# Optimization experiments

Measured on AMD Instinct MI355X. Metric: run time of the kernel, lower is better.

Reference implementation:

```python
import jax, jax.numpy as jnp
import numpy as np

N, E, H, ED = 20000, 320000, 256, 64  # nodes, edges, hidden_dim, edge_feature_dim


def setup_inputs() -> dict:
    key = jax.random.key(0)
    ks = jax.random.split(key, 12)

    def init_w(k, shape, fan_in):
        return (jax.random.normal(k, shape, jnp.float32) / np.sqrt(fan_in)).astype(jnp.float32)

    h = jax.random.normal(ks[0], (N, H), jnp.float32)
    edge_indices = jax.random.randint(ks[1], (2, E), 0, N, jnp.int32)
    edge_attr = jax.random.normal(ks[2], (E, ED), jnp.float32)

    din = 2 * H + ED  # edge_network input: [h[row], h[col], edge_attr]
    W1 = init_w(ks[3], (H, din), din)
    b1 = jnp.zeros((H,), jnp.float32)
    W2 = init_w(ks[4], (H, H), H)
    b2 = jnp.zeros((H,), jnp.float32)
    # GRUCell params, gate order (r, z, n) as in torch
    W_ih = init_w(ks[5], (3 * H, H), H)
    b_ih = jnp.zeros((3 * H,), jnp.float32)
    W_hh = init_w(ks[6], (3 * H, H), H)
    b_hh = jnp.zeros((3 * H,), jnp.float32)

    return {"h": h, "edge_indices": edge_indices, "edge_attr": edge_attr,
            "W1": W1, "b1": b1, "W2": W2, "b2": b2,
            "W_ih": W_ih, "b_ih": b_ih, "W_hh": W_hh, "b_hh": b_hh}


def reference(h, edge_indices, edge_attr, W1, b1, W2, b2, W_ih, b_ih, W_hh, b_hh):
    row, col = edge_indices[0], edge_indices[1]
    # message: edge_network MLP on [h[row], h[col], edge_attr]
    edge_in = jnp.concatenate([h[row], h[col], edge_attr], axis=-1)  # [E, 2H+ED]
    msg = jax.nn.relu(edge_in @ W1.T + b1) @ W2.T + b2               # [E, H]
    # scatter_add aggregation by destination node (row)
    agg = jax.ops.segment_sum(msg, row, num_segments=h.shape[0])     # [N, H]
    # GRUCell update: input=agg, hidden=h
    gx = agg @ W_ih.T + b_ih
    gh = h @ W_hh.T + b_hh
    xr, xz, xn = jnp.split(gx, 3, axis=-1)
    hr, hz, hn = jnp.split(gh, 3, axis=-1)
    r = jax.nn.sigmoid(xr + hr)
    z = jax.nn.sigmoid(xz + hz)
    n = jnp.tanh(xn + r * hn)
    h_new = (1.0 - z) * n + z * h
    return h_new  # dropout p=0.0 -> identity
```

## Files before the change

kernel.cpp:

```cpp
#include <hip/hip_runtime.h>
#include <math.h>

#define NN 20000
#define NE 320000
#define HD 256
#define EDIM 64
#define DIN 576
#define ASTRIDE 264

typedef __attribute__((ext_vector_type(4))) _Float16 h4;
typedef __attribute__((ext_vector_type(8))) _Float16 h8;
typedef __attribute__((ext_vector_type(4))) float f32x4;

__device__ _Float16 g_W1cf[16 * 2 * 64 * 8];
__device__ _Float16 g_W12f[32 * 8 * 64 * 8];
__device__ _Float16 g_Wrzf[32 * 16 * 64 * 8];
__device__ _Float16 g_Wnxf[16 * 8 * 64 * 8];
__device__ _Float16 g_Wnhf[16 * 8 * 64 * 8];
__device__ float    g_Wib2[768];
__device__ _Float16 g_pre[(size_t)NN * 512];
__device__ _Float16 g_hf[(size_t)NN * 256];
__device__ int      g_rowptr[NN + 1];
__device__ int      g_cursor[NN];
__device__ int      g_perm[NE];
__device__ int      g_prow[NE];
__device__ int      g_pcol[NE];

__device__ __forceinline__ h4 f2h4(float4 v) {
  return (h4){(_Float16)v.x, (_Float16)v.y, (_Float16)v.z, (_Float16)v.w};
}
__device__ __forceinline__ h8 f2h8(float4 a, float4 b) {
  return (h8){(_Float16)a.x, (_Float16)a.y, (_Float16)a.z, (_Float16)a.w,
              (_Float16)b.x, (_Float16)b.y, (_Float16)b.z, (_Float16)b.w};
}

__global__ __launch_bounds__(256) void cvtfold_kernel(
    const float* __restrict__ W1, const float* __restrict__ W_hh,
    const float* __restrict__ W_ih, const float* __restrict__ W2,
    const float* __restrict__ b2)
{
  const int bid = blockIdx.x;
  if (bid < 768) {
    const int r = bid, c = threadIdx.x;
    const float* wr = W_ih + (size_t)r * HD;
    float acc = 0.f;
    for (int m = 0; m < HD; ++m) acc += wr[m] * W2[(size_t)m * HD + c];
    const int ks = c >> 5, lg = (c >> 3) & 3, j = c & 7;
    const int l = lg * 16 + (r & 15);
    if (r < 512) {
      const int cf = (r < 256) ? (r >> 4) : (16 + ((r - 256) >> 4));
      g_Wrzf[(size_t)((cf * 16 + ks) * 64 + l) * 8 + j] = (_Float16)acc;
    } else {
      const int cf = (r - 512) >> 4;
      g_Wnxf[(size_t)((cf * 8 + ks) * 64 + l) * 8 + j] = (_Float16)acc;
    }
    if (c == 0) {
      float a2 = 0.f;
      for (int m = 0; m < HD; ++m) a2 += wr[m] * b2[m];
      g_Wib2[r] = a2;
    }
    return;
  }
  const int idx = (bid - 768) * 256 + threadIdx.x;
  const int g = idx >> 6, l = idx & 63;
  const int r16 = l & 15, koff = (l >> 4) * 8;
  const float* src; _Float16* dst;
  if (g < 32) {
    const int cf = g >> 1, ks = g & 1;
    src = &W1[(size_t)(cf * 16 + r16) * DIN + 512 + ks * 32 + koff];
    dst = &g_W1cf[(size_t)(cf * 2 + ks) * 512 + l * 8];
  } else if (g < 288) {
    const int gg = g - 32, cf = gg >> 3, ks = gg & 7;
    src = (cf < 16) ? &W1[(size_t)(cf * 16 + r16) * DIN + ks * 32 + koff]
                    : &W1[(size_t)((cf - 16) * 16 + r16) * DIN + 256 + ks * 32 + koff];
    dst = &g_W12f[(size_t)(cf * 8 + ks) * 512 + l * 8];
  } else if (g < 544) {
    const int gg = g - 288, cf = gg >> 3, ks = 8 + (gg & 7);
    const int row = (cf < 16) ? cf * 16 + r16 : 256 + (cf - 16) * 16 + r16;
    src = &W_hh[(size_t)row * HD + (ks - 8) * 32 + koff];
    dst = &g_Wrzf[(size_t)(cf * 16 + ks) * 512 + l * 8];
  } else {
    const int gg = g - 544, cf = gg >> 3, ks = gg & 7;
    src = &W_hh[(size_t)(512 + cf * 16 + r16) * HD + ks * 32 + koff];
    dst = &g_Wnhf[(size_t)(cf * 8 + ks) * 512 + l * 8];
  }
#pragma unroll
  for (int j = 0; j < 8; ++j) dst[j] = (_Float16)src[j];
}

#define PSTR 264
__global__ __launch_bounds__(256, 4) void pre_kernel(const float* __restrict__ h,
                                                     const int* __restrict__ ei,
                                                     int* __restrict__ deg) {
  __shared__ _Float16 A[32 * PSTR];
  const int t = threadIdx.x, w = t >> 6, l = t & 63;
  const int l15 = l & 15, lg = l >> 4;
  const int nb = blockIdx.x * 32;

  {
    const int gid = blockIdx.x * 256 + t;
    atomicAdd(&deg[ei[gid]], 1);
    atomicAdd(&deg[ei[gid + NE / 2]], 1);
  }

  const int row = t >> 3, c8 = t & 7;
#pragma unroll
  for (int i = 0; i < 8; ++i) {
    const int col4 = c8 + i * 8;
    float4 v = ((const float4*)(h + (size_t)(nb + row) * HD))[col4];
    const h4 x = f2h4(v);
    *(h4*)&A[row * PSTR + col4 * 4] = x;
    *(h4*)&g_hf[(size_t)(nb + row) * 256 + col4 * 4] = x;
  }
  __syncthreads();

  f32x4 acc[2][8];
#pragma unroll
  for (int m = 0; m < 2; ++m)
#pragma unroll
    for (int n = 0; n < 8; ++n) acc[m][n] = (f32x4){0.f, 0.f, 0.f, 0.f};

  for (int ks = 0; ks < 8; ++ks) {
    h8 a[2];
#pragma unroll
    for (int m = 0; m < 2; ++m)
      a[m] = *(const h8*)&A[(m * 16 + l15) * PSTR + ks * 32 + lg * 8];
#pragma unroll
    for (int n = 0; n < 8; ++n) {
      const h8 b = *(const h8*)&g_W12f[(size_t)((w * 8 + n) * 8 + ks) * 512 + l * 8];
#pragma unroll
      for (int m = 0; m < 2; ++m)
        acc[m][n] = __builtin_amdgcn_mfma_f32_16x16x32_f16(a[m], b, acc[m][n], 0, 0, 0);
    }
  }

#pragma unroll
  for (int m = 0; m < 2; ++m)
#pragma unroll
    for (int n = 0; n < 8; ++n) {
      const int col = w * 128 + n * 16 + l15;
#pragma unroll
      for (int r = 0; r < 4; ++r)
        g_pre[(size_t)(nb + m * 16 + lg * 4 + r) * 512 + col] = (_Float16)acc[m][n][r];
    }
}

__global__ __launch_bounds__(512) void scan_kernel(const int* __restrict__ deg) {
  __shared__ int part[512];
  const int t = threadIdx.x;
  const int base = t * 40;
  int loc[40];
  int s = 0;
#pragma unroll
  for (int i = 0; i < 40; ++i) {
    const int idx = base + i;
    const int d = (idx < NN) ? deg[idx] : 0;
    loc[i] = s; s += d;
  }
  part[t] = s;
  __syncthreads();
  for (int off = 1; off < 512; off <<= 1) {
    const int v = (t >= off) ? part[t - off] : 0;
    __syncthreads();
    part[t] += v;
    __syncthreads();
  }
  const int pre = (t == 0) ? 0 : part[t - 1];
#pragma unroll
  for (int i = 0; i < 40; ++i) {
    const int idx = base + i;
    if (idx < NN) { const int v = pre + loc[i]; g_rowptr[idx] = v; g_cursor[idx] = v; }
  }
  if (t == 511) g_rowptr[NN] = part[511];
}

__global__ __launch_bounds__(256) void scatter_kernel(const int* __restrict__ ei) {
  const int e = blockIdx.x * 256 + threadIdx.x;
  if (e < NE) {
    const int r = ei[e];
    const int p = atomicAdd(&g_cursor[r], 1);
    g_perm[p] = e;
    g_prow[p] = r;
    g_pcol[p] = ei[NE + e];
  }
}

__global__ __launch_bounds__(256, 4) void aggmsg_kernel(const float* __restrict__ eattr,
                                                        const float* __restrict__ b1,
                                                        float* __restrict__ S32) {
  __shared__ _Float16 T[64 * ASTRIDE];
  const int t = threadIdx.x, w = t >> 6, l = t & 63;
  const int l15 = l & 15, lg = l >> 4;
  const int p0 = blockIdx.x * 64;

  int pe[4];
#pragma unroll
  for (int m = 0; m < 4; ++m) pe[m] = g_perm[p0 + m * 16 + l15];

  f32x4 acc[4][4];
#pragma unroll
  for (int m = 0; m < 4; ++m)
#pragma unroll
    for (int n = 0; n < 4; ++n) acc[m][n] = (f32x4){0.f, 0.f, 0.f, 0.f};

#pragma unroll
  for (int ks = 0; ks < 2; ++ks) {
    h8 a[4], b[4];
#pragma unroll
    for (int m = 0; m < 4; ++m) {
      const float* ep = eattr + (size_t)pe[m] * EDIM + ks * 32 + lg * 8;
      a[m] = f2h8(((const float4*)ep)[0], ((const float4*)ep)[1]);
    }
#pragma unroll
    for (int n = 0; n < 4; ++n)
      b[n] = *(const h8*)&g_W1cf[(size_t)((w * 4 + n) * 2 + ks) * 512 + l * 8];
#pragma unroll
    for (int m = 0; m < 4; ++m)
#pragma unroll
      for (int n = 0; n < 4; ++n)
        acc[m][n] = __builtin_amdgcn_mfma_f32_16x16x32_f16(a[m], b[n], acc[m][n], 0, 0, 0);
  }

#pragma unroll
  for (int m = 0; m < 4; ++m)
#pragma unroll
    for (int n = 0; n < 4; ++n)
#pragma unroll
      for (int r = 0; r < 4; ++r)
        T[(m * 16 + lg * 4 + r) * ASTRIDE + w * 64 + n * 16 + l15] = (_Float16)acc[m][n][r];
  __syncthreads();

  const f32x4 b1v = *(const f32x4*)&b1[l * 4];
  int cur = -1;
  f32x4 sum = (f32x4){0.f, 0.f, 0.f, 0.f};
#pragma unroll
  for (int i = 0; i < 16; ++i) {
    const int p = p0 + w * 16 + i;
    const int node = g_prow[p];
    const int src  = g_pcol[p];
    const h4 tt = *(const h4*)&T[(w * 16 + i) * ASTRIDE + l * 4];
    const h4 q1 = *(const h4*)&g_pre[(size_t)node * 512 + l * 4];
    const h4 q2 = *(const h4*)&g_pre[(size_t)src * 512 + 256 + l * 4];
    f32x4 v;
#pragma unroll
    for (int r = 0; r < 4; ++r) {
      float x = (float)tt[r] + (float)q1[r] + (float)q2[r] + b1v[r];
      v[r] = x > 0.f ? x : 0.f;
    }
    if (node != cur) {
      if (cur >= 0) {
#pragma unroll
        for (int r = 0; r < 4; ++r) unsafeAtomicAdd(&S32[(size_t)cur * HD + l * 4 + r], sum[r]);
      }
      cur = node; sum = v;
    } else {
#pragma unroll
      for (int r = 0; r < 4; ++r) sum[r] += v[r];
    }
  }
#pragma unroll
  for (int r = 0; r < 4; ++r) unsafeAtomicAdd(&S32[(size_t)cur * HD + l * 4 + r], sum[r]);
}

__global__ __launch_bounds__(256, 2) void node_kernel(
    const float* __restrict__ S32,
    const float* __restrict__ b_ih, const float* __restrict__ b_hh,
    float* __restrict__ out)
{
  const int bid = blockIdx.x;
  const int cf = bid & 3, rng = bid >> 2;
  const int t = threadIdx.x, w = t >> 6, l = t & 63;
  const int l15 = l & 15, lg = l >> 4;
  const int nb = rng * 64;
  const int cf0 = cf * 4;
  int na = nb + w * 16 + l15; if (na >= NN) na = NN - 1;

  f32x4 ar[4], az[4], ax[4], ah[4];
#pragma unroll
  for (int n = 0; n < 4; ++n) {
    ar[n] = (f32x4){0.f, 0.f, 0.f, 0.f}; az[n] = (f32x4){0.f, 0.f, 0.f, 0.f};
    ax[n] = (f32x4){0.f, 0.f, 0.f, 0.f}; ah[n] = (f32x4){0.f, 0.f, 0.f, 0.f};
  }

  const float* aS = &S32[(size_t)na * 256 + lg * 8];
  const _Float16* aH = &g_hf[(size_t)na * 256 + lg * 8];

#pragma unroll
  for (int ks = 0; ks < 8; ++ks) {
    const float4 s0 = ((const float4*)&aS[ks * 32])[0];
    const float4 s1 = ((const float4*)&aS[ks * 32])[1];
    const h8 a = f2h8(s0, s1);
    h8 br[4], bz[4], bn[4];
#pragma unroll
    for (int n = 0; n < 4; ++n) {
      br[n] = *(const h8*)&g_Wrzf[(size_t)(((cf0 + n) * 16 + ks) * 64 + l) * 8];
      bz[n] = *(const h8*)&g_Wrzf[(size_t)(((16 + cf0 + n) * 16 + ks) * 64 + l) * 8];
      bn[n] = *(const h8*)&g_Wnxf[(size_t)(((cf0 + n) * 8 + ks) * 64 + l) * 8];
    }
#pragma unroll
    for (int n = 0; n < 4; ++n) {
      ar[n] = __builtin_amdgcn_mfma_f32_16x16x32_f16(a, br[n], ar[n], 0, 0, 0);
      az[n] = __builtin_amdgcn_mfma_f32_16x16x32_f16(a, bz[n], az[n], 0, 0, 0);
      ax[n] = __builtin_amdgcn_mfma_f32_16x16x32_f16(a, bn[n], ax[n], 0, 0, 0);
    }
  }

#pragma unroll
  for (int ks = 0; ks < 8; ++ks) {
    const h8 a = *(const h8*)&aH[ks * 32];
    h8 br[4], bz[4], bn[4];
#pragma unroll
    for (int n = 0; n < 4; ++n) {
      br[n] = *(const h8*)&g_Wrzf[(size_t)(((cf0 + n) * 16 + 8 + ks) * 64 + l) * 8];
      bz[n] = *(const h8*)&g_Wrzf[(size_t)(((16 + cf0 + n) * 16 + 8 + ks) * 64 + l) * 8];
      bn[n] = *(const h8*)&g_Wnhf[(size_t)(((cf0 + n) * 8 + ks) * 64 + l) * 8];
    }
#pragma unroll
    for (int n = 0; n < 4; ++n) {
      ar[n] = __builtin_amdgcn_mfma_f32_16x16x32_f16(a, br[n], ar[n], 0, 0, 0);
      az[n] = __builtin_amdgcn_mfma_f32_16x16x32_f16(a, bz[n], az[n], 0, 0, 0);
      ah[n] = __builtin_amdgcn_mfma_f32_16x16x32_f16(a, bn[n], ah[n], 0, 0, 0);
    }
  }

#pragma unroll
  for (int r = 0; r < 4; ++r) {
    const int node = nb + w * 16 + lg * 4 + r;
    if (node >= NN) continue;
    const float df = (float)(g_rowptr[node + 1] - g_rowptr[node]);
#pragma unroll
    for (int n = 0; n < 4; ++n) {
      const int c = cf * 64 + n * 16 + l15;
      const float rg = 1.f / (1.f + __expf(-(ar[n][r] + df * g_Wib2[c] + b_ih[c] + b_hh[c])));
      const float zg = 1.f / (1.f + __expf(-(az[n][r] + df * g_Wib2[HD + c] + b_ih[HD + c] + b_hh[HD + c])));
      const float u  = ax[n][r] + df * g_Wib2[2 * HD + c] + b_ih[2 * HD + c]
                       + rg * (ah[n][r] + b_hh[2 * HD + c]);
      const float eu = __expf(2.f * fabsf(u));
      const float ng = copysignf(1.f - 2.f / (eu + 1.f), u);
      const float hv = (float)g_hf[(size_t)node * 256 + c];
      out[(size_t)node * HD + c] = (1.f - zg) * ng + zg * hv;
    }
  }
}

extern "C" void kernel_launch(void* const* d_in, const int* in_sizes, int n_in,
                              void* d_out, int out_size, void* d_ws, size_t ws_size,
                              hipStream_t stream)
{
  const float* h     = (const float*)d_in[0];
  const int*   ei    = (const int*)d_in[1];
  const float* eattr = (const float*)d_in[2];
  const float* W1    = (const float*)d_in[3];
  const float* b1    = (const float*)d_in[4];
  const float* W2    = (const float*)d_in[5];
  const float* b2    = (const float*)d_in[6];
  const float* W_ih  = (const float*)d_in[7];
  const float* b_ih  = (const float*)d_in[8];
  const float* W_hh  = (const float*)d_in[9];
  const float* b_hh  = (const float*)d_in[10];
  float* out = (float*)d_out;

  float* S32 = (float*)d_ws;
  int*   deg = (int*)((char*)d_ws + (size_t)NN * HD * 4);

  hipMemsetAsync(d_ws, 0, (size_t)NN * HD * 4 + (size_t)NN * 4, stream);
  cvtfold_kernel<<<768 + 168, 256, 0, stream>>>(W1, W_hh, W_ih, W2, b2);
  pre_kernel<<<NN / 32, 256, 0, stream>>>(h, ei, deg);
  scan_kernel<<<1, 512, 0, stream>>>(deg);
  scatter_kernel<<<(NE + 255) / 256, 256, 0, stream>>>(ei);
  aggmsg_kernel<<<NE / 64, 256, 0, stream>>>(eattr, b1, S32);
  node_kernel<<<1252, 256, 0, stream>>>(S32, b_ih, b_hh, out);
}
```

Before: 326.1 us.

## Pre-permute edge attributes to fp16 in scatter; load q1 once per node segment

The scatter kernel is replaced by a perm kernel that, besides building the CSR permutation, writes edge_attr converted to fp16 in sorted order into a new global buffer. The aggregation kernel then reads contiguous fp16 rows instead of gathering fp32 rows through a perm index. The row-node projection q1 is now loaded only when the destination node changes, not once per edge. This adds an extra write and read of the fp16 edge-attribute copy, about 41MB each way, and fewer threads per edge in the scatter step.

```diff
diff --git a/kernel.cpp b/kernel.cpp
--- a/kernel.cpp
+++ b/kernel.cpp
@@ -20,9 +20,9 @@
 __device__ float    g_Wib2[768];
 __device__ _Float16 g_pre[(size_t)NN * 512];
 __device__ _Float16 g_hf[(size_t)NN * 256];
+__device__ _Float16 g_ea16[(size_t)NE * EDIM];
 __device__ int      g_rowptr[NN + 1];
 __device__ int      g_cursor[NN];
-__device__ int      g_perm[NE];
 __device__ int      g_prow[NE];
 __device__ int      g_pcol[NE];
 
@@ -174,29 +174,36 @@
   if (t == 511) g_rowptr[NN] = part[511];
 }
 
-__global__ __launch_bounds__(256) void scatter_kernel(const int* __restrict__ ei) {
-  const int e = blockIdx.x * 256 + threadIdx.x;
-  if (e < NE) {
-    const int r = ei[e];
-    const int p = atomicAdd(&g_cursor[r], 1);
-    g_perm[p] = e;
-    g_prow[p] = r;
-    g_pcol[p] = ei[NE + e];
-  }
-}
-
-__global__ __launch_bounds__(256, 4) void aggmsg_kernel(const float* __restrict__ eattr,
-                                                        const float* __restrict__ b1,
+__global__ __launch_bounds__(256) void perm_kernel(const float* __restrict__ eattr,
+                                                   const int* __restrict__ ei) {
+  __shared__ int pL[64];
+  const int t = threadIdx.x, w = t >> 6, l = t & 63;
+  const int e0 = blockIdx.x * 64;
+
+  if (t < 64) {
+    const int dest = ei[e0 + t];
+    const int p = atomicAdd(&g_cursor[dest], 1);
+    pL[t] = p;
+    g_prow[p] = dest;
+    g_pcol[p] = ei[NE + e0 + t];
+  }
+  __syncthreads();
+
+#pragma unroll
+  for (int i = 0; i < 16; ++i) {
+    const int e = e0 + w * 16 + i;
+    const float v = eattr[(size_t)e * EDIM + l];
+    g_ea16[(size_t)pL[w * 16 + i] * EDIM + l] = (_Float16)v;
+  }
+}
+
+__global__ __launch_bounds__(256, 4) void aggmsg_kernel(const float* __restrict__ b1,
                                                         float* __restrict__ S32) {
   __shared__ _Float16 T[64 * ASTRIDE];
   const int t = threadIdx.x, w = t >> 6, l = t & 63;
   const int l15 = l & 15, lg = l >> 4;
   const int p0 = blockIdx.x * 64;
 
-  int pe[4];
-#pragma unroll
-  for (int m = 0; m < 4; ++m) pe[m] = g_perm[p0 + m * 16 + l15];
-
   f32x4 acc[4][4];
 #pragma unroll
   for (int m = 0; m < 4; ++m)
@@ -207,10 +214,8 @@
   for (int ks = 0; ks < 2; ++ks) {
     h8 a[4], b[4];
 #pragma unroll
-    for (int m = 0; m < 4; ++m) {
-      const float* ep = eattr + (size_t)pe[m] * EDIM + ks * 32 + lg * 8;
-      a[m] = f2h8(((const float4*)ep)[0], ((const float4*)ep)[1]);
-    }
+    for (int m = 0; m < 4; ++m)
+      a[m] = *(const h8*)&g_ea16[(size_t)(p0 + m * 16 + l15) * EDIM + ks * 32 + lg * 8];
 #pragma unroll
     for (int n = 0; n < 4; ++n)
       b[n] = *(const h8*)&g_W1cf[(size_t)((w * 4 + n) * 2 + ks) * 512 + l * 8];
@@ -232,34 +237,34 @@
 
   const f32x4 b1v = *(const f32x4*)&b1[l * 4];
   int cur = -1;
+  h4 q1 = (h4){0, 0, 0, 0};
   f32x4 sum = (f32x4){0.f, 0.f, 0.f, 0.f};
 #pragma unroll
   for (int i = 0; i < 16; ++i) {
     const int p = p0 + w * 16 + i;
     const int node = g_prow[p];
     const int src  = g_pcol[p];
-    const h4 tt = *(const h4*)&T[(w * 16 + i) * ASTRIDE + l * 4];
-    const h4 q1 = *(const h4*)&g_pre[(size_t)node * 512 + l * 4];
-    const h4 q2 = *(const h4*)&g_pre[(size_t)src * 512 + 256 + l * 4];
-    f32x4 v;
-#pragma unroll
-    for (int r = 0; r < 4; ++r) {
-      float x = (float)tt[r] + (float)q1[r] + (float)q2[r] + b1v[r];
-      v[r] = x > 0.f ? x : 0.f;
-    }
     if (node != cur) {
       if (cur >= 0) {
 #pragma unroll
-        for (int r = 0; r < 4; ++r) unsafeAtomicAdd(&S32[(size_t)cur * HD + l * 4 + r], sum[r]);
+        for (int r = 0; r < 4; ++r)
+          unsafeAtomicAdd(&S32[(size_t)cur * HD + l * 4 + r], sum[r]);
       }
-      cur = node; sum = v;
-    } else {
-#pragma unroll
-      for (int r = 0; r < 4; ++r) sum[r] += v[r];
-    }
-  }
-#pragma unroll
-  for (int r = 0; r < 4; ++r) unsafeAtomicAdd(&S32[(size_t)cur * HD + l * 4 + r], sum[r]);
+      cur = node;
+      sum = (f32x4){0.f, 0.f, 0.f, 0.f};
+      q1 = *(const h4*)&g_pre[(size_t)node * 512 + l * 4];
+    }
+    const h4 tt = *(const h4*)&T[(w * 16 + i) * ASTRIDE + l * 4];
+    const h4 q2 = *(const h4*)&g_pre[(size_t)src * 512 + 256 + l * 4];
+#pragma unroll
+    for (int r = 0; r < 4; ++r) {
+      const float x = (float)tt[r] + (float)q1[r] + (float)q2[r] + b1v[r];
+      sum[r] += x > 0.f ? x : 0.f;
+    }
+  }
+#pragma unroll
+  for (int r = 0; r < 4; ++r)
+    unsafeAtomicAdd(&S32[(size_t)cur * HD + l * 4 + r], sum[r]);
 }
 
 __global__ __launch_bounds__(256, 2) void node_kernel(
@@ -367,7 +372,7 @@
   cvtfold_kernel<<<768 + 168, 256, 0, stream>>>(W1, W_hh, W_ih, W2, b2);
   pre_kernel<<<NN / 32, 256, 0, stream>>>(h, ei, deg);
   scan_kernel<<<1, 512, 0, stream>>>(deg);
-  scatter_kernel<<<(NE + 255) / 256, 256, 0, stream>>>(ei);
-  aggmsg_kernel<<<NE / 64, 256, 0, stream>>>(eattr, b1, S32);
+  perm_kernel<<<NE / 64, 256, 0, stream>>>(eattr, ei);
+  aggmsg_kernel<<<NE / 64, 256, 0, stream>>>(b1, S32);
   node_kernel<<<1252, 256, 0, stream>>>(S32, b_ih, b_hh, out);
 }
```

New measurement: 329.7 us. No clear change (+1.1%).
